# Kernel tuning notes

Hardware: AMD Instinct MI355X
Metric: run time of the kernel (lower is better)

Reference implementation:

```python
import jax, jax.numpy as jnp
import numpy as np

H = 1024        # bridge_hidden_dim
NH = 16         # num_attention_heads
HD = H // NH    # head_dim = 64
B, S = 4, 1024
PHYS_W = 0.2
CONS_W = 0.15


def setup_inputs() -> dict:
    key = jax.random.key(0)
    ks = jax.random.split(key, 16)
    sc = 0.02
    return {
        "cnn_features": jax.random.normal(ks[0], (B, S, H), jnp.float32),
        "llm_features": jax.random.normal(ks[1], (B, S, H), jnp.float32),
        "Wq": jax.random.normal(ks[2], (H, H), jnp.float32) * sc,
        "bq": jnp.zeros((H,), jnp.float32),
        "Wk": jax.random.normal(ks[3], (H, H), jnp.float32) * sc,
        "bk": jnp.zeros((H,), jnp.float32),
        "Wv": jax.random.normal(ks[4], (H, H), jnp.float32) * sc,
        "bv": jnp.zeros((H,), jnp.float32),
        "Wo": jax.random.normal(ks[5], (H, H), jnp.float32) * sc,
        "bo": jnp.zeros((H,), jnp.float32),
        "ln_g": jnp.ones((H,), jnp.float32),
        "ln_b": jnp.zeros((H,), jnp.float32),
        "e_energy": jax.random.normal(ks[6], (H,), jnp.float32),
        "e_mass": jax.random.normal(ks[7], (H,), jnp.float32),
        "e_momentum": jax.random.normal(ks[8], (H,), jnp.float32),
    }


def _layernorm(x, g, b, eps=1e-5):
    mu = jnp.mean(x, axis=-1, keepdims=True)
    var = jnp.var(x, axis=-1, keepdims=True)
    return (x - mu) * jax.lax.rsqrt(var + eps) * g + b


def _split_heads(x):
    b, s, _ = x.shape
    return x.reshape(b, s, NH, HD).transpose(0, 2, 1, 3)  # [b, h, s, d]


def _physics_attention(q_in, k_in, v_in, Wq, bq, Wk, bk, Wv, bv, Wo, bo, ln_g, ln_b):
    # q_in: [b, sq, H]; k_in == v_in: [b, sk, H] with sq == sk (required by bias math)
    Q = _split_heads(q_in @ Wq.T + bq)  # [b,h,s,d]
    K = _split_heads(k_in @ Wk.T + bk)
    V = _split_heads(v_in @ Wv.T + bv)
    scores = jnp.einsum('bhqd,bhkd->bhqk', Q, K) / jnp.sqrt(jnp.float32(HD))
    # physics constraints (broadcast [b,h,s,1] over key axis)
    energy_bias = jnp.sum(Q * K, axis=-1, keepdims=True) * PHYS_W
    mass_bias = jnp.mean(Q + K, axis=-1, keepdims=True) * CONS_W
    scores = scores + energy_bias + mass_bias
    attn = jax.nn.softmax(scores, axis=-1)  # dropout is identity in eval
    att = jnp.einsum('bhqk,bhkd->bhqd', attn, V)
    b, h, s, d = att.shape
    att = att.transpose(0, 2, 1, 3).reshape(b, s, h * d)
    out = att @ Wo.T + bo
    return _layernorm(q_in + out, ln_g, ln_b)


def reference(cnn_features, llm_features, Wq, bq, Wk, bk, Wv, bv, Wo, bo,
              ln_g, ln_b, e_energy, e_mass, e_momentum):
    b = cnn_features.shape[0]
    phys = jnp.stack([e_energy, e_mass, e_momentum], axis=0)  # [3, H]
    phys = jnp.broadcast_to(phys[None], (b, 3, H))
    aug_cnn = jnp.concatenate([cnn_features, phys], axis=1)  # [b, S+3, H]
    aug_llm = jnp.concatenate([llm_features, phys], axis=1)
    cnn_att = _physics_attention(aug_cnn, aug_llm, aug_llm,
                                 Wq, bq, Wk, bk, Wv, bv, Wo, bo, ln_g, ln_b)
    llm_att = _physics_attention(aug_llm, aug_cnn, aug_cnn,
                                 Wq, bq, Wk, bk, Wv, bv, Wo, bo, ln_g, ln_b)
    cnn_out = cnn_att[:, :cnn_features.shape[1], :]
    llm_out = llm_att[:, :llm_features.shape[1], :]
    return (cnn_out, llm_out)
```

## Files before the change

### kernel.cpp

```cpp
#include <hip/hip_runtime.h>
#include <stdint.h>

#define SA 1027
#define SPAD 1088

typedef __attribute__((ext_vector_type(8))) short short8;
typedef __attribute__((ext_vector_type(4))) float f32x4;
typedef __attribute__((ext_vector_type(2))) unsigned int u32x2;

typedef const __attribute__((address_space(1))) uint8_t* gas1;
typedef __attribute__((address_space(3))) uint8_t* las3;

__device__ __forceinline__ void gload16(const void* g, void* l){
  __builtin_amdgcn_global_load_lds((gas1)g, (las3)l, 16, 0, 0);
}

__device__ __forceinline__ uint16_t f2bf(float f){
  uint32_t x = __builtin_bit_cast(uint32_t, f);
  x = (x + 0x7fffu + ((x >> 16) & 1u)) >> 16;
  return (uint16_t)x;
}
__device__ __forceinline__ float bf2f(uint16_t u){
  uint32_t x = ((uint32_t)u) << 16;
  return __builtin_bit_cast(float, x);
}

__device__ __forceinline__ f32x4 mfma16(short8 a, short8 b, f32x4 c){
  return __builtin_amdgcn_mfma_f32_16x16x32_bf16(a, b, c, 0, 0, 0);
}

#define QSCALE 0.18033688011112042f

__global__ __launch_bounds__(256) void prep_wb(
    const float* __restrict__ Wq, const float* __restrict__ Wk,
    const float* __restrict__ Wv, const float* __restrict__ Wo,
    const float* __restrict__ bq, const float* __restrict__ bk,
    const float* __restrict__ bv, const float* __restrict__ bo,
    uint16_t* __restrict__ W, float* __restrict__ bias){
  const int gid = blockIdx.x*256 + threadIdx.x;
  if (gid < 1048576){
    const int w = gid >> 18;
    const int off = (gid & 262143) << 2;
    const float* src = (w==0) ? Wq : (w==1) ? Wk : (w==2) ? Wv : Wo;
    const float4 v = *(const float4*)(src + off);
    ushort4 u;
    u.x = f2bf(v.x); u.y = f2bf(v.y); u.z = f2bf(v.z); u.w = f2bf(v.w);
    *(ushort4*)(W + ((size_t)w << 20) + off) = u;
  } else if (gid < 1048576 + 1024){
    const int i = (gid - 1048576) << 2;
    const int w = i >> 10;
    const int off = i & 1023;
    const float* src = (w==0) ? bq : (w==1) ? bk : (w==2) ? bv : bo;
    *(float4*)(bias + i) = *(const float4*)(src + off);
  }
}

__global__ __launch_bounds__(256) void prep_X(
    const float* __restrict__ cnn, const float* __restrict__ llm,
    uint16_t* __restrict__ X){
  const int row = blockIdx.x*2 + (threadIdx.x >> 7);
  const int c8 = (threadIdx.x & 127) << 3;
  const int cb = row >> 10, s = row & 1023;
  const int c = cb >> 2, b = cb & 3;
  const float* src = (c ? llm : cnn) + ((size_t)(b*1024 + s))*1024 + c8;
  const float4 v0 = *(const float4*)src;
  const float4 v1 = *(const float4*)(src + 4);
  short8 u;
  u[0]=(short)f2bf(v0.x); u[1]=(short)f2bf(v0.y); u[2]=(short)f2bf(v0.z); u[3]=(short)f2bf(v0.w);
  u[4]=(short)f2bf(v1.x); u[5]=(short)f2bf(v1.y); u[6]=(short)f2bf(v1.z); u[7]=(short)f2bf(v1.w);
  *(short8*)(X + (size_t)row*1024 + c8) = u;
}

__global__ __launch_bounds__(256) void phys_qkv(
    const float* __restrict__ ee, const float* __restrict__ em,
    const float* __restrict__ ep, const uint16_t* __restrict__ W,
    const float* __restrict__ bias, uint16_t* __restrict__ Yqk,
    uint16_t* __restrict__ Vt){
  __shared__ float xs[1024];
  const int t = blockIdx.x >> 3;
  const int col = 1024 + (blockIdx.x & 7)*256 + threadIdx.x;
  const float* e = (t==0) ? ee : (t==1) ? em : ep;
  for (int k = threadIdx.x; k < 1024; k += 256) xs[k] = bf2f(f2bf(e[k]));
  __syncthreads();
  const uint16_t* wr = W + (size_t)col*1024;
  float acc = 0.f;
  for (int k = 0; k < 1024; k += 8){
    const short8 w8 = *(const short8*)(wr + k);
    #pragma unroll
    for (int u = 0; u < 8; ++u) acc += bf2f((uint16_t)w8[u]) * xs[k+u];
  }
  const uint16_t o = f2bf(acc + bias[col]);
  if (col < 2048){
    #pragma unroll
    for (int cb = 0; cb < 8; ++cb)
      Yqk[((size_t)cb*SA + 1024 + t)*2048 + col] = o;
  } else {
    const int hd = col - 2048;
    #pragma unroll
    for (int cb = 0; cb < 8; ++cb)
      Vt[((size_t)(cb*1024 + hd))*SPAD + 1024 + t] = o;
  }
}

__global__ __launch_bounds__(512, 2) void qkv192(
    const uint16_t* __restrict__ A, const uint16_t* __restrict__ B,
    const float* __restrict__ bias, uint16_t* __restrict__ Yqk,
    uint16_t* __restrict__ Vt){
  extern __shared__ uint8_t lds[];
  const int tid = threadIdx.x;
  const int lane = tid & 63, wid = tid >> 6;
  const int l15 = lane & 15, l4 = lane >> 4;
  const int wm = wid >> 2, wn = wid & 3;
  const int wg = (blockIdx.x & 7)*64 + (blockIdx.x >> 3);
  const int bm = wg >> 4, bn = wg & 15;

  const uint16_t* Ag = A + (size_t)bm*256*1024;
  const uint16_t* Bg = B + (size_t)bn*192*1024;

  const int srow8 = lane >> 3;
  const int gch = (lane & 7) ^ srow8;
  const int c0 = wid*2, c1 = c0 + 1;
  const size_t ga0 = (size_t)(c0*8 + srow8)*1024 + gch*8;
  const size_t ga1 = (size_t)(c1*8 + srow8)*1024 + gch*8;
  const size_t gb0 = (size_t)((wid*3+0)*8 + srow8)*1024 + gch*8;
  const size_t gb1 = (size_t)((wid*3+1)*8 + srow8)*1024 + gch*8;
  const size_t gb2 = (size_t)((wid*3+2)*8 + srow8)*1024 + gch*8;

#define STG_A(buf, H, kt) do { \
    gload16(Ag + (size_t)(H)*131072 + (size_t)(kt)*64 + ga0, lds + (buf)*57344 + (H)*16384 + c0*1024); \
    gload16(Ag + (size_t)(H)*131072 + (size_t)(kt)*64 + ga1, lds + (buf)*57344 + (H)*16384 + c1*1024); \
  } while(0)
#define STG_B(buf, kt) do { \
    gload16(Bg + (size_t)(kt)*64 + gb0, lds + (buf)*57344 + 32768 + (wid*3+0)*1024); \
    gload16(Bg + (size_t)(kt)*64 + gb1, lds + (buf)*57344 + 32768 + (wid*3+1)*1024); \
    gload16(Bg + (size_t)(kt)*64 + gb2, lds + (buf)*57344 + 32768 + (wid*3+2)*1024); \
  } while(0)

  int koff[2];
  koff[0] = (l4*16) ^ ((l15 & 7) << 4);
  koff[1] = (64 + l4*16) ^ ((l15 & 7) << 4);
  const int arow = (wm*128 + l15) * 128;
  const int bbase = 32768 + (wn*48 + l15) * 128;

  f32x4 acc[8][3];
  #pragma unroll
  for (int i = 0; i < 8; ++i)
    #pragma unroll
    for (int j = 0; j < 3; ++j) acc[i][j] = (f32x4){0.f,0.f,0.f,0.f};

  const int NT = 16;
  STG_A(0,0,0); STG_A(0,1,0); STG_B(0,0); STG_B(1,1);
  asm volatile("s_waitcnt vmcnt(3)" ::: "memory");
  __builtin_amdgcn_s_barrier();

  for (int s = 0; s < NT; ++s){
    const int b = s & 1, nb = b ^ 1;
    const uint8_t* L = lds + b*57344;
    short8 af[4][2], af2[4][2], bfr[3][2];

    if (s+1 < NT){ STG_A(nb, 0, s+1); STG_A(nb, 1, s+1); }
    #pragma unroll
    for (int i = 0; i < 4; ++i){
      af[i][0] = *(const short8*)(L + arow + i*2048 + koff[0]);
      af[i][1] = *(const short8*)(L + arow + i*2048 + koff[1]);
    }
    #pragma unroll
    for (int j = 0; j < 3; ++j){
      bfr[j][0] = *(const short8*)(L + bbase + j*2048 + koff[0]);
      bfr[j][1] = *(const short8*)(L + bbase + j*2048 + koff[1]);
    }
    __builtin_amdgcn_s_barrier();
    asm volatile("s_waitcnt lgkmcnt(0)" ::: "memory");
    __builtin_amdgcn_s_setprio(1);
    #pragma unroll
    for (int i = 0; i < 4; ++i)
      #pragma unroll
      for (int j = 0; j < 3; ++j)
        acc[i][j] = mfma16(af[i][1], bfr[j][1], mfma16(af[i][0], bfr[j][0], acc[i][j]));
    __builtin_amdgcn_s_setprio(0);
    __builtin_amdgcn_s_barrier();

    if (s+2 < NT){ STG_B(b, s+2); }
    #pragma unroll
    for (int i = 0; i < 4; ++i){
      af2[i][0] = *(const short8*)(L + arow + 8192 + i*2048 + koff[0]);
      af2[i][1] = *(const short8*)(L + arow + 8192 + i*2048 + koff[1]);
    }
    __builtin_amdgcn_s_barrier();
    asm volatile("s_waitcnt lgkmcnt(0)" ::: "memory");
    __builtin_amdgcn_s_setprio(1);
    #pragma unroll
    for (int i = 0; i < 4; ++i)
      #pragma unroll
      for (int j = 0; j < 3; ++j)
        acc[i+4][j] = mfma16(af2[i][1], bfr[j][1], mfma16(af2[i][0], bfr[j][0], acc[i+4][j]));
    __builtin_amdgcn_s_setprio(0);
    if (s < NT-2)       asm volatile("s_waitcnt vmcnt(3)" ::: "memory");
    else if (s == NT-2) asm volatile("s_waitcnt vmcnt(0)" ::: "memory");
    __builtin_amdgcn_s_barrier();
  }

  #pragma unroll
  for (int j = 0; j < 3; ++j){
    const int n = bn*192 + wn*48 + j*16 + l15;
    const float bb = bias[n];
    if (n < 2048){
      const float sc = (n < 1024) ? QSCALE : 1.0f;
      #pragma unroll
      for (int i = 0; i < 8; ++i){
        const int m0 = bm*256 + wm*128 + i*16 + l4*4;
        #pragma unroll
        for (int r = 0; r < 4; ++r){
          const int m = m0 + r;
          Yqk[((size_t)(m >> 10)*SA + (m & 1023))*2048 + n] = f2bf((acc[i][j][r] + bb) * sc);
        }
      }
    } else {
      const int hd = n - 2048;
      #pragma unroll
      for (int i = 0; i < 8; ++i){
        const int m0 = bm*256 + wm*128 + i*16 + l4*4;
        const size_t vrow = (size_t)(m0 >> 10)*1024 + hd;
        const uint32_t w0 = (uint32_t)f2bf(acc[i][j][0] + bb) | ((uint32_t)f2bf(acc[i][j][1] + bb) << 16);
        const uint32_t w1 = (uint32_t)f2bf(acc[i][j][2] + bb) | ((uint32_t)f2bf(acc[i][j][3] + bb) << 16);
        *(u32x2*)(Vt + vrow*SPAD + (m0 & 1023)) = (u32x2){w0, w1};
      }
    }
  }
#undef STG_A
#undef STG_B
}

__global__ __launch_bounds__(512, 2) void oproj256(
    const uint16_t* __restrict__ A, const uint16_t* __restrict__ B,
    const float* __restrict__ bias, uint16_t* __restrict__ C){
  extern __shared__ uint8_t lds[];
  const int tid = threadIdx.x;
  const int lane = tid & 63, wid = tid >> 6;
  const int l15 = lane & 15, l4 = lane >> 4;
  const int wm = wid >> 2, wn = wid & 3;
  const int wg = (blockIdx.x & 7)*32 + (blockIdx.x >> 3);
  const int bm = wg >> 3, bn = wg & 7;

  const uint16_t* Ag = A + (size_t)bm*256*1024;
  const uint16_t* Bg = B + (size_t)bn*128*1024;

  const int srow8 = lane >> 3;
  const int gch = (lane & 7) ^ srow8;
  const int c0 = wid*2, c1 = c0 + 1;
  const size_t ga0 = (size_t)(c0*8 + srow8)*1024 + gch*8;
  const size_t ga1 = (size_t)(c1*8 + srow8)*1024 + gch*8;

#define STG_A(buf, H, kt) do { \
    gload16(Ag + (size_t)(H)*131072 + (size_t)(kt)*64 + ga0, lds + (buf)*49152 + (H)*16384 + c0*1024); \
    gload16(Ag + (size_t)(H)*131072 + (size_t)(kt)*64 + ga1, lds + (buf)*49152 + (H)*16384 + c1*1024); \
  } while(0)
#define STG_B(buf, kt) do { \
    gload16(Bg + (size_t)(kt)*64 + ga0, lds + (buf)*49152 + 32768 + c0*1024); \
    gload16(Bg + (size_t)(kt)*64 + ga1, lds + (buf)*49152 + 32768 + c1*1024); \
  } while(0)

  int koff[2];
  koff[0] = (l4*16) ^ ((l15 & 7) << 4);
  koff[1] = (64 + l4*16) ^ ((l15 & 7) << 4);
  const int abase = wm*16384 + l15*128;
  const int bbase = 32768 + (wn*32 + l15)*128;

  f32x4 acc[8][2];
  #pragma unroll
  for (int i = 0; i < 8; ++i){ acc[i][0] = (f32x4){0,0,0,0}; acc[i][1] = (f32x4){0,0,0,0}; }

  const int NT = 16;
  STG_A(0,0,0); STG_A(0,1,0); STG_B(0,0); STG_B(1,1);
  asm volatile("s_waitcnt vmcnt(2)" ::: "memory");
  __builtin_amdgcn_s_barrier();

  for (int s = 0; s < NT; ++s){
    const int b = s & 1, nb = b ^ 1;
    const uint8_t* L = lds + b*49152;
    short8 af[4][2], af2[4][2], bfr[2][2];

    if (s+1 < NT){ STG_A(nb, 0, s+1); }
    #pragma unroll
    for (int i = 0; i < 4; ++i){
      af[i][0] = *(const short8*)(L + abase + i*2048 + koff[0]);
      af[i][1] = *(const short8*)(L + abase + i*2048 + koff[1]);
    }
    #pragma unroll
    for (int j = 0; j < 2; ++j){
      bfr[j][0] = *(const short8*)(L + bbase + j*2048 + koff[0]);
      bfr[j][1] = *(const short8*)(L + bbase + j*2048 + koff[1]);
    }
    __builtin_amdgcn_s_barrier();
    asm volatile("s_waitcnt lgkmcnt(0)" ::: "memory");
    __builtin_amdgcn_s_setprio(1);
    #pragma unroll
    for (int i = 0; i < 4; ++i)
      #pragma unroll
      for (int j = 0; j < 2; ++j)
        acc[i][j] = mfma16(af[i][1], bfr[j][1], mfma16(af[i][0], bfr[j][0], acc[i][j]));
    __builtin_amdgcn_s_setprio(0);
    __builtin_amdgcn_s_barrier();

    if (s+1 < NT){ STG_A(nb, 1, s+1); }
    if (s+2 < NT){ STG_B(b, s+2); }
    #pragma unroll
    for (int i = 0; i < 4; ++i){
      af2[i][0] = *(const short8*)(L + abase + 8192 + i*2048 + koff[0]);
      af2[i][1] = *(const short8*)(L + abase + 8192 + i*2048 + koff[1]);
    }
    __builtin_amdgcn_s_barrier();
    asm volatile("s_waitcnt lgkmcnt(0)" ::: "memory");
    __builtin_amdgcn_s_setprio(1);
    #pragma unroll
    for (int i = 0; i < 4; ++i)
      #pragma unroll
      for (int j = 0; j < 2; ++j)
        acc[i+4][j] = mfma16(af2[i][1], bfr[j][1], mfma16(af2[i][0], bfr[j][0], acc[i+4][j]));
    __builtin_amdgcn_s_setprio(0);
    if (s < NT-2)       asm volatile("s_waitcnt vmcnt(2)" ::: "memory");
    else if (s == NT-2) asm volatile("s_waitcnt vmcnt(0)" ::: "memory");
    __builtin_amdgcn_s_barrier();
  }

  #pragma unroll
  for (int j = 0; j < 2; ++j){
    const int n = bn*128 + wn*32 + j*16 + l15;
    const float bb = bias[n];
    #pragma unroll
    for (int i = 0; i < 8; ++i){
      const size_t m0 = (size_t)bm*256 + wm*128 + i*16 + l4*4;
      #pragma unroll
      for (int r = 0; r < 4; ++r)
        C[(m0 + r)*1024 + n] = f2bf(acc[i][j][r] + bb);
    }
  }
#undef STG_A
#undef STG_B
}

__global__ __launch_bounds__(512, 4) void attn_k(
    const uint16_t* __restrict__ Yqk, const uint16_t* __restrict__ Vt,
    uint16_t* __restrict__ att){
  extern __shared__ uint8_t lds[];
  const int tid = threadIdx.x;
  const int lane = tid & 63, wid = tid >> 6;
  const int l15 = lane & 15, l4 = lane >> 4;
  const int i = blockIdx.x;
  const int inst = (i & 7)*16 + ((i >> 3) & 15);
  const int qb = i >> 7;
  const int h = inst & 15, cb = inst >> 4;
  const size_t yrow0 = (size_t)cb * SA;
  const int q0 = qb*256 + wid*32;
  const size_t vbase = (size_t)inst * 64 * SPAD;
  const uint16_t* Yk = Yqk + yrow0*2048 + 1024 + h*64;

  short8 qf[2][2];
  #pragma unroll
  for (int u = 0; u < 2; ++u){
    const uint16_t* p = Yqk + (yrow0 + q0 + u*16 + l15)*2048 + h*64 + l4*8;
    qf[u][0] = *(const short8*)p;
    qf[u][1] = *(const short8*)(p + 32);
  }

  f32x4 o0[4], o1[4];
  float psum0 = 0.f, psum1 = 0.f;
  #pragma unroll
  for (int d = 0; d < 4; ++d){ o0[d] = (f32x4){0,0,0,0}; o1[d] = (f32x4){0,0,0,0}; }

  int koff[2], koffp[2], pwo[4];
  #pragma unroll
  for (int kk = 0; kk < 2; ++kk){
    koff[kk]  = (l15*128 + kk*64 + l4*16) ^ ((l15 & 7) << 4);
    koffp[kk] = l15*144 + kk*64 + l4*16;
  }
  #pragma unroll
  for (int nt = 0; nt < 4; ++nt)
    pwo[nt] = l15*144 + nt*32 + l4*8;
  uint8_t* const pb = lds + 49152 + wid*2304;

  const int srow = lane >> 3, schunk = lane & 7;
  const int strow = wid*8 + srow;
  const int sgch = schunk ^ srow;

#define ASTAGE(t3, kt) do { \
    gload16(Yk + (size_t)((kt)*64 + strow)*2048 + sgch*8, lds + (t3)*8192 + wid*1024); \
    gload16(Vt + vbase + (size_t)strow*SPAD + (kt)*64 + sgch*8, lds + 24576 + (t3)*8192 + wid*1024); \
  } while(0)

  ASTAGE(0, 0);
  ASTAGE(1, 1);
  asm volatile("s_waitcnt vmcnt(2)" ::: "memory");
  __builtin_amdgcn_s_barrier();

  for (int kt = 0; kt < 17; ++kt){
    const int c3 = kt % 3;
    if (kt <= 14){ const int t3 = (kt + 2) % 3; ASTAGE(t3, kt + 2); }
    const uint8_t* bK = lds + c3*8192;
    const uint8_t* bV = lds + 24576 + c3*8192;

    f32x4 sa[4], sb[4];
    #pragma unroll
    for (int nt = 0; nt < 4; ++nt){
      const short8 k0 = *(const short8*)(bK + nt*2048 + koff[0]);
      const short8 k1 = *(const short8*)(bK + nt*2048 + koff[1]);
      sa[nt] = mfma16(k1, qf[0][1], mfma16(k0, qf[0][0], (f32x4){0,0,0,0}));
      sb[nt] = mfma16(k1, qf[1][1], mfma16(k0, qf[1][0], (f32x4){0,0,0,0}));
    }
    if (kt == 16){
      #pragma unroll
      for (int nt = 0; nt < 4; ++nt)
        #pragma unroll
        for (int r = 0; r < 4; ++r){
          if (nt*16 + l4*4 + r >= 3){ sa[nt][r] = -3e38f; sb[nt][r] = -3e38f; }
        }
    }
    #pragma unroll
    for (int nt = 0; nt < 4; ++nt){
      const float p0 = __builtin_amdgcn_exp2f(sa[nt][0]);
      const float p1 = __builtin_amdgcn_exp2f(sa[nt][1]);
      const float p2 = __builtin_amdgcn_exp2f(sa[nt][2]);
      const float p3 = __builtin_amdgcn_exp2f(sa[nt][3]);
      psum0 += (p0 + p1) + (p2 + p3);
      uint32_t w0, w1;
      asm("v_cvt_pk_bf16_f32 %0, %1, %2" : "=v"(w0) : "v"(p0), "v"(p1));
      asm("v_cvt_pk_bf16_f32 %0, %1, %2" : "=v"(w1) : "v"(p2), "v"(p3));
      *(u32x2*)(pb + pwo[nt]) = (u32x2){w0, w1};
    }
    short8 vf[4][2];
    #pragma unroll
    for (int dt = 0; dt < 4; ++dt){
      vf[dt][0] = *(const short8*)(bV + dt*2048 + koff[0]);
      vf[dt][1] = *(const short8*)(bV + dt*2048 + koff[1]);
    }
    #pragma unroll
    for (int kk = 0; kk < 2; ++kk){
      const short8 pf = *(const short8*)(pb + koffp[kk]);
      #pragma unroll
      for (int dt = 0; dt < 4; ++dt)
        o0[dt] = mfma16(pf, vf[dt][kk], o0[dt]);
    }
    #pragma unroll
    for (int nt = 0; nt < 4; ++nt){
      const float p0 = __builtin_amdgcn_exp2f(sb[nt][0]);
      const float p1 = __builtin_amdgcn_exp2f(sb[nt][1]);
      const float p2 = __builtin_amdgcn_exp2f(sb[nt][2]);
      const float p3 = __builtin_amdgcn_exp2f(sb[nt][3]);
      psum1 += (p0 + p1) + (p2 + p3);
      uint32_t w0, w1;
      asm("v_cvt_pk_bf16_f32 %0, %1, %2" : "=v"(w0) : "v"(p0), "v"(p1));
      asm("v_cvt_pk_bf16_f32 %0, %1, %2" : "=v"(w1) : "v"(p2), "v"(p3));
      *(u32x2*)(pb + pwo[nt]) = (u32x2){w0, w1};
    }
    #pragma unroll
    for (int kk = 0; kk < 2; ++kk){
      const short8 pf = *(const short8*)(pb + koffp[kk]);
      #pragma unroll
      for (int dt = 0; dt < 4; ++dt)
        o1[dt] = mfma16(pf, vf[dt][kk], o1[dt]);
    }
    if (kt <= 14)      asm volatile("s_waitcnt vmcnt(2)" ::: "memory");
    else if (kt == 15) asm volatile("s_waitcnt vmcnt(0)" ::: "memory");
    if (kt <= 15) __builtin_amdgcn_s_barrier();
  }
#undef ASTAGE

  psum0 += __shfl_xor(psum0, 16); psum0 += __shfl_xor(psum0, 32);
  psum1 += __shfl_xor(psum1, 16); psum1 += __shfl_xor(psum1, 32);
  const size_t arow0 = (size_t)cb*1024 + q0;
  #pragma unroll
  for (int r = 0; r < 4; ++r){
    const float inv0 = 1.f / __shfl(psum0, l4*4 + r);
    const float inv1 = 1.f / __shfl(psum1, l4*4 + r);
    #pragma unroll
    for (int dt = 0; dt < 4; ++dt){
      att[(arow0 + l4*4 + r)*1024 + h*64 + dt*16 + l15] = f2bf(o0[dt][r] * inv0);
      att[(arow0 + 16 + l4*4 + r)*1024 + h*64 + dt*16 + l15] = f2bf(o1[dt][r] * inv1);
    }
  }
}

__global__ __launch_bounds__(256) void ln_out(
    const uint16_t* __restrict__ Op, const float* __restrict__ cnn,
    const float* __restrict__ llm, const float* __restrict__ g,
    const float* __restrict__ b, float* __restrict__ out){
  const int row = blockIdx.x;
  const int c = row >> 12, bq = row & 4095;
  const int tid = threadIdx.x;
  const ushort4 u = *(const ushort4*)(Op + (size_t)row*1024 + (tid<<2));
  const float4 rv = *(const float4*)((c ? llm : cnn) + (size_t)bq*1024 + (tid<<2));
  const float x0 = bf2f(u.x) + rv.x;
  const float x1 = bf2f(u.y) + rv.y;
  const float x2 = bf2f(u.z) + rv.z;
  const float x3 = bf2f(u.w) + rv.w;
  float s1 = x0+x1+x2+x3;
  float s2 = x0*x0+x1*x1+x2*x2+x3*x3;
  #pragma unroll
  for (int m=1;m<64;m<<=1){ s1 += __shfl_xor(s1,m); s2 += __shfl_xor(s2,m); }
  __shared__ float r1[4], r2[4];
  const int wid = tid >> 6, lane = tid & 63;
  if (lane == 0){ r1[wid] = s1; r2[wid] = s2; }
  __syncthreads();
  s1 = r1[0]+r1[1]+r1[2]+r1[3];
  s2 = r2[0]+r2[1]+r2[2]+r2[3];
  const float mu = s1 * 0.0009765625f;
  const float var = s2 * 0.0009765625f - mu*mu;
  const float rs = rsqrtf(var + 1e-5f);
  const float4 gv = *(const float4*)(g + (tid<<2));
  const float4 bv = *(const float4*)(b + (tid<<2));
  float4 ov;
  ov.x = (x0 - mu)*rs*gv.x + bv.x;
  ov.y = (x1 - mu)*rs*gv.y + bv.y;
  ov.z = (x2 - mu)*rs*gv.z + bv.z;
  ov.w = (x3 - mu)*rs*gv.w + bv.w;
  *(float4*)(out + ((size_t)c << 22) + (size_t)bq*1024 + (tid<<2)) = ov;
}

extern "C" void kernel_launch(void* const* d_in, const int* in_sizes, int n_in,
                              void* d_out, int out_size, void* d_ws, size_t ws_size,
                              hipStream_t stream){
  const float* cnn = (const float*)d_in[0];
  const float* llm = (const float*)d_in[1];
  const float* Wq  = (const float*)d_in[2];
  const float* bq  = (const float*)d_in[3];
  const float* Wk  = (const float*)d_in[4];
  const float* bk  = (const float*)d_in[5];
  const float* Wv  = (const float*)d_in[6];
  const float* bv  = (const float*)d_in[7];
  const float* Wo  = (const float*)d_in[8];
  const float* bo  = (const float*)d_in[9];
  const float* lng = (const float*)d_in[10];
  const float* lnb = (const float*)d_in[11];
  const float* ee  = (const float*)d_in[12];
  const float* em  = (const float*)d_in[13];
  const float* ep  = (const float*)d_in[14];

  uint8_t* ws = (uint8_t*)d_ws;
  uint16_t* X    = (uint16_t*)(ws + 0);
  uint16_t* W    = (uint16_t*)(ws + 16777216);
  float*    bias = (float*)   (ws + 25165824);
  uint16_t* Yqk  = (uint16_t*)(ws + 25182208);
  uint16_t* Vt   = (uint16_t*)(ws + 59785216);
  uint16_t* att  = X;
  uint16_t* Op   = Yqk;
  float* out = (float*)d_out;

  hipFuncSetAttribute((const void*)qkv192,
                      hipFuncAttributeMaxDynamicSharedMemorySize, 114688);
  hipFuncSetAttribute((const void*)oproj256,
                      hipFuncAttributeMaxDynamicSharedMemorySize, 98304);
  hipFuncSetAttribute((const void*)attn_k,
                      hipFuncAttributeMaxDynamicSharedMemorySize, 67584);

  prep_wb<<<4100, 256, 0, stream>>>(Wq, Wk, Wv, Wo, bq, bk, bv, bo, W, bias);
  prep_X<<<4096, 256, 0, stream>>>(cnn, llm, X);
  phys_qkv<<<24, 256, 0, stream>>>(ee, em, ep, W, bias, Yqk, Vt);
  qkv192<<<512, 512, 114688, stream>>>(X, W, bias, Yqk, Vt);
  attn_k<<<512, 512, 67584, stream>>>(Yqk, Vt, att);
  oproj256<<<256, 512, 98304, stream>>>(att, W + 3145728, bias + 3072, Op);
  ln_out<<<8192, 256, 0, stream>>>(Op, cnn, llm, lng, lnb, out);
}
```

Measured before the change: 175.5 us.

## Merge prep kernels into one launch and halve GEMM M-tiles to 128 rows

Combines weight conversion, input conversion and the physics-token QKV projection into a single prep kernel. The physics projection now reads fp32 weights directly, so it no longer depends on the converted bf16 weights. The QKV and output-projection GEMMs shrink their M tile from 256 to 128 rows, which halves LDS and accumulator use so launch bounds can target 4 blocks per CU, and doubles the grid. This trades fewer launches and higher occupancy for less operand reuse per tile and more global traffic for the B matrix.

```diff
diff --git a/kernel.cpp b/kernel.cpp
--- a/kernel.cpp
+++ b/kernel.cpp
@@ -31,78 +31,80 @@
 
 #define QSCALE 0.18033688011112042f
 
-__global__ __launch_bounds__(256) void prep_wb(
+__global__ __launch_bounds__(256) void prep_all(
+    const float* __restrict__ cnn, const float* __restrict__ llm,
     const float* __restrict__ Wq, const float* __restrict__ Wk,
     const float* __restrict__ Wv, const float* __restrict__ Wo,
     const float* __restrict__ bq, const float* __restrict__ bk,
     const float* __restrict__ bv, const float* __restrict__ bo,
-    uint16_t* __restrict__ W, float* __restrict__ bias){
-  const int gid = blockIdx.x*256 + threadIdx.x;
-  if (gid < 1048576){
-    const int w = gid >> 18;
-    const int off = (gid & 262143) << 2;
-    const float* src = (w==0) ? Wq : (w==1) ? Wk : (w==2) ? Wv : Wo;
-    const float4 v = *(const float4*)(src + off);
-    ushort4 u;
-    u.x = f2bf(v.x); u.y = f2bf(v.y); u.z = f2bf(v.z); u.w = f2bf(v.w);
-    *(ushort4*)(W + ((size_t)w << 20) + off) = u;
-  } else if (gid < 1048576 + 1024){
-    const int i = (gid - 1048576) << 2;
-    const int w = i >> 10;
-    const int off = i & 1023;
-    const float* src = (w==0) ? bq : (w==1) ? bk : (w==2) ? bv : bo;
-    *(float4*)(bias + i) = *(const float4*)(src + off);
-  }
-}
-
-__global__ __launch_bounds__(256) void prep_X(
-    const float* __restrict__ cnn, const float* __restrict__ llm,
-    uint16_t* __restrict__ X){
-  const int row = blockIdx.x*2 + (threadIdx.x >> 7);
-  const int c8 = (threadIdx.x & 127) << 3;
-  const int cb = row >> 10, s = row & 1023;
-  const int c = cb >> 2, b = cb & 3;
-  const float* src = (c ? llm : cnn) + ((size_t)(b*1024 + s))*1024 + c8;
-  const float4 v0 = *(const float4*)src;
-  const float4 v1 = *(const float4*)(src + 4);
-  short8 u;
-  u[0]=(short)f2bf(v0.x); u[1]=(short)f2bf(v0.y); u[2]=(short)f2bf(v0.z); u[3]=(short)f2bf(v0.w);
-  u[4]=(short)f2bf(v1.x); u[5]=(short)f2bf(v1.y); u[6]=(short)f2bf(v1.z); u[7]=(short)f2bf(v1.w);
-  *(short8*)(X + (size_t)row*1024 + c8) = u;
-}
-
-__global__ __launch_bounds__(256) void phys_qkv(
     const float* __restrict__ ee, const float* __restrict__ em,
-    const float* __restrict__ ep, const uint16_t* __restrict__ W,
-    const float* __restrict__ bias, uint16_t* __restrict__ Yqk,
+    const float* __restrict__ ep,
+    uint16_t* __restrict__ W, float* __restrict__ bias,
+    uint16_t* __restrict__ X, uint16_t* __restrict__ Yqk,
     uint16_t* __restrict__ Vt){
-  __shared__ float xs[1024];
-  const int t = blockIdx.x >> 3;
-  const int col = 1024 + (blockIdx.x & 7)*256 + threadIdx.x;
-  const float* e = (t==0) ? ee : (t==1) ? em : ep;
-  for (int k = threadIdx.x; k < 1024; k += 256) xs[k] = bf2f(f2bf(e[k]));
-  __syncthreads();
-  const uint16_t* wr = W + (size_t)col*1024;
-  float acc = 0.f;
-  for (int k = 0; k < 1024; k += 8){
-    const short8 w8 = *(const short8*)(wr + k);
-    #pragma unroll
-    for (int u = 0; u < 8; ++u) acc += bf2f((uint16_t)w8[u]) * xs[k+u];
-  }
-  const uint16_t o = f2bf(acc + bias[col]);
-  if (col < 2048){
-    #pragma unroll
-    for (int cb = 0; cb < 8; ++cb)
-      Yqk[((size_t)cb*SA + 1024 + t)*2048 + col] = o;
+  const int bid = blockIdx.x;
+  if (bid < 4100){
+    const int gid = bid*256 + threadIdx.x;
+    if (gid < 1048576){
+      const int w = gid >> 18;
+      const int off = (gid & 262143) << 2;
+      const float* src = (w==0) ? Wq : (w==1) ? Wk : (w==2) ? Wv : Wo;
+      const float4 v = *(const float4*)(src + off);
+      ushort4 u;
+      u.x = f2bf(v.x); u.y = f2bf(v.y); u.z = f2bf(v.z); u.w = f2bf(v.w);
+      *(ushort4*)(W + ((size_t)w << 20) + off) = u;
+    } else if (gid < 1048576 + 1024){
+      const int i = (gid - 1048576) << 2;
+      const int w = i >> 10;
+      const int off = i & 1023;
+      const float* src = (w==0) ? bq : (w==1) ? bk : (w==2) ? bv : bo;
+      *(float4*)(bias + i) = *(const float4*)(src + off);
+    }
+  } else if (bid < 8196){
+    const int rb = bid - 4100;
+    const int row = rb*2 + (threadIdx.x >> 7);
+    const int c8 = (threadIdx.x & 127) << 3;
+    const int cb = row >> 10, s = row & 1023;
+    const int c = cb >> 2, b = cb & 3;
+    const float* src = (c ? llm : cnn) + ((size_t)(b*1024 + s))*1024 + c8;
+    const float4 v0 = *(const float4*)src;
+    const float4 v1 = *(const float4*)(src + 4);
+    short8 u;
+    u[0]=(short)f2bf(v0.x); u[1]=(short)f2bf(v0.y); u[2]=(short)f2bf(v0.z); u[3]=(short)f2bf(v0.w);
+    u[4]=(short)f2bf(v1.x); u[5]=(short)f2bf(v1.y); u[6]=(short)f2bf(v1.z); u[7]=(short)f2bf(v1.w);
+    *(short8*)(X + (size_t)row*1024 + c8) = u;
   } else {
-    const int hd = col - 2048;
-    #pragma unroll
-    for (int cb = 0; cb < 8; ++cb)
-      Vt[((size_t)(cb*1024 + hd))*SPAD + 1024 + t] = o;
-  }
-}
-
-__global__ __launch_bounds__(512, 2) void qkv192(
+    __shared__ float xs[1024];
+    const int pb = bid - 8196;
+    const int t = pb >> 3;
+    const int col = 1024 + (pb & 7)*256 + threadIdx.x;
+    const float* e = (t==0) ? ee : (t==1) ? em : ep;
+    for (int k = threadIdx.x; k < 1024; k += 256) xs[k] = bf2f(f2bf(e[k]));
+    __syncthreads();
+    const float* wrow = (col < 2048) ? (Wk + (size_t)(col-1024)*1024)
+                                     : (Wv + (size_t)(col-2048)*1024);
+    const float bb = (col < 2048) ? bk[col-1024] : bv[col-2048];
+    float acc = 0.f;
+    for (int k = 0; k < 1024; k += 4){
+      const float4 w4 = *(const float4*)(wrow + k);
+      acc += bf2f(f2bf(w4.x))*xs[k] + bf2f(f2bf(w4.y))*xs[k+1]
+           + bf2f(f2bf(w4.z))*xs[k+2] + bf2f(f2bf(w4.w))*xs[k+3];
+    }
+    const uint16_t o = f2bf(acc + bb);
+    if (col < 2048){
+      #pragma unroll
+      for (int cb = 0; cb < 8; ++cb)
+        Yqk[((size_t)cb*SA + 1024 + t)*2048 + col] = o;
+    } else {
+      const int hd = col - 2048;
+      #pragma unroll
+      for (int cb = 0; cb < 8; ++cb)
+        Vt[((size_t)(cb*1024 + hd))*SPAD + 1024 + t] = o;
+    }
+  }
+}
+
+__global__ __launch_bounds__(512, 4) void qkv128(
     const uint16_t* __restrict__ A, const uint16_t* __restrict__ B,
     const float* __restrict__ bias, uint16_t* __restrict__ Yqk,
     uint16_t* __restrict__ Vt){
@@ -111,10 +113,10 @@
   const int lane = tid & 63, wid = tid >> 6;
   const int l15 = lane & 15, l4 = lane >> 4;
   const int wm = wid >> 2, wn = wid & 3;
-  const int wg = (blockIdx.x & 7)*64 + (blockIdx.x >> 3);
+  const int wg = (blockIdx.x & 7)*128 + (blockIdx.x >> 3);
   const int bm = wg >> 4, bn = wg & 15;
 
-  const uint16_t* Ag = A + (size_t)bm*256*1024;
+  const uint16_t* Ag = A + (size_t)bm*128*1024;
   const uint16_t* Bg = B + (size_t)bn*192*1024;
 
   const int srow8 = lane >> 3;
@@ -126,41 +128,41 @@
   const size_t gb1 = (size_t)((wid*3+1)*8 + srow8)*1024 + gch*8;
   const size_t gb2 = (size_t)((wid*3+2)*8 + srow8)*1024 + gch*8;
 
-#define STG_A(buf, H, kt) do { \
-    gload16(Ag + (size_t)(H)*131072 + (size_t)(kt)*64 + ga0, lds + (buf)*57344 + (H)*16384 + c0*1024); \
-    gload16(Ag + (size_t)(H)*131072 + (size_t)(kt)*64 + ga1, lds + (buf)*57344 + (H)*16384 + c1*1024); \
+#define STG_A(buf, kt) do { \
+    gload16(Ag + (size_t)(kt)*64 + ga0, lds + (buf)*40960 + c0*1024); \
+    gload16(Ag + (size_t)(kt)*64 + ga1, lds + (buf)*40960 + c1*1024); \
   } while(0)
 #define STG_B(buf, kt) do { \
-    gload16(Bg + (size_t)(kt)*64 + gb0, lds + (buf)*57344 + 32768 + (wid*3+0)*1024); \
-    gload16(Bg + (size_t)(kt)*64 + gb1, lds + (buf)*57344 + 32768 + (wid*3+1)*1024); \
-    gload16(Bg + (size_t)(kt)*64 + gb2, lds + (buf)*57344 + 32768 + (wid*3+2)*1024); \
+    gload16(Bg + (size_t)(kt)*64 + gb0, lds + (buf)*40960 + 16384 + (wid*3+0)*1024); \
+    gload16(Bg + (size_t)(kt)*64 + gb1, lds + (buf)*40960 + 16384 + (wid*3+1)*1024); \
+    gload16(Bg + (size_t)(kt)*64 + gb2, lds + (buf)*40960 + 16384 + (wid*3+2)*1024); \
   } while(0)
 
   int koff[2];
   koff[0] = (l4*16) ^ ((l15 & 7) << 4);
   koff[1] = (64 + l4*16) ^ ((l15 & 7) << 4);
-  const int arow = (wm*128 + l15) * 128;
-  const int bbase = 32768 + (wn*48 + l15) * 128;
-
-  f32x4 acc[8][3];
-  #pragma unroll
-  for (int i = 0; i < 8; ++i)
+  const int arow = (wm*64 + l15) * 128;
+  const int bbase = 16384 + (wn*48 + l15) * 128;
+
+  f32x4 acc[4][3];
+  #pragma unroll
+  for (int i = 0; i < 4; ++i)
     #pragma unroll
     for (int j = 0; j < 3; ++j) acc[i][j] = (f32x4){0.f,0.f,0.f,0.f};
 
   const int NT = 16;
-  STG_A(0,0,0); STG_A(0,1,0); STG_B(0,0); STG_B(1,1);
+  STG_A(0,0); STG_B(0,0); STG_B(1,1);
   asm volatile("s_waitcnt vmcnt(3)" ::: "memory");
   __builtin_amdgcn_s_barrier();
 
   for (int s = 0; s < NT; ++s){
     const int b = s & 1, nb = b ^ 1;
-    const uint8_t* L = lds + b*57344;
-    short8 af[4][2], af2[4][2], bfr[3][2];
-
-    if (s+1 < NT){ STG_A(nb, 0, s+1); STG_A(nb, 1, s+1); }
-    #pragma unroll
-    for (int i = 0; i < 4; ++i){
+    const uint8_t* L = lds + b*40960;
+    short8 af[2][2], af2[2][2], bfr[3][2];
+
+    if (s+1 < NT){ STG_A(nb, s+1); }
+    #pragma unroll
+    for (int i = 0; i < 2; ++i){
       af[i][0] = *(const short8*)(L + arow + i*2048 + koff[0]);
       af[i][1] = *(const short8*)(L + arow + i*2048 + koff[1]);
     }
@@ -173,7 +175,7 @@
     asm volatile("s_waitcnt lgkmcnt(0)" ::: "memory");
     __builtin_amdgcn_s_setprio(1);
     #pragma unroll
-    for (int i = 0; i < 4; ++i)
+    for (int i = 0; i < 2; ++i)
       #pragma unroll
       for (int j = 0; j < 3; ++j)
         acc[i][j] = mfma16(af[i][1], bfr[j][1], mfma16(af[i][0], bfr[j][0], acc[i][j]));
@@ -182,18 +184,18 @@
 
     if (s+2 < NT){ STG_B(b, s+2); }
     #pragma unroll
-    for (int i = 0; i < 4; ++i){
-      af2[i][0] = *(const short8*)(L + arow + 8192 + i*2048 + koff[0]);
-      af2[i][1] = *(const short8*)(L + arow + 8192 + i*2048 + koff[1]);
+    for (int i = 0; i < 2; ++i){
+      af2[i][0] = *(const short8*)(L + arow + 4096 + i*2048 + koff[0]);
+      af2[i][1] = *(const short8*)(L + arow + 4096 + i*2048 + koff[1]);
     }
     __builtin_amdgcn_s_barrier();
     asm volatile("s_waitcnt lgkmcnt(0)" ::: "memory");
     __builtin_amdgcn_s_setprio(1);
     #pragma unroll
-    for (int i = 0; i < 4; ++i)
+    for (int i = 0; i < 2; ++i)
       #pragma unroll
       for (int j = 0; j < 3; ++j)
-        acc[i+4][j] = mfma16(af2[i][1], bfr[j][1], mfma16(af2[i][0], bfr[j][0], acc[i+4][j]));
+        acc[i+2][j] = mfma16(af2[i][1], bfr[j][1], mfma16(af2[i][0], bfr[j][0], acc[i+2][j]));
     __builtin_amdgcn_s_setprio(0);
     if (s < NT-2)       asm volatile("s_waitcnt vmcnt(3)" ::: "memory");
     else if (s == NT-2) asm volatile("s_waitcnt vmcnt(0)" ::: "memory");
@@ -207,8 +209,8 @@
     if (n < 2048){
       const float sc = (n < 1024) ? QSCALE : 1.0f;
       #pragma unroll
-      for (int i = 0; i < 8; ++i){
-        const int m0 = bm*256 + wm*128 + i*16 + l4*4;
+      for (int i = 0; i < 4; ++i){
+        const int m0 = bm*128 + wm*64 + i*16 + l4*4;
         #pragma unroll
         for (int r = 0; r < 4; ++r){
           const int m = m0 + r;
@@ -218,8 +220,8 @@
     } else {
       const int hd = n - 2048;
       #pragma unroll
-      for (int i = 0; i < 8; ++i){
-        const int m0 = bm*256 + wm*128 + i*16 + l4*4;
+      for (int i = 0; i < 4; ++i){
+        const int m0 = bm*128 + wm*64 + i*16 + l4*4;
         const size_t vrow = (size_t)(m0 >> 10)*1024 + hd;
         const uint32_t w0 = (uint32_t)f2bf(acc[i][j][0] + bb) | ((uint32_t)f2bf(acc[i][j][1] + bb) << 16);
         const uint32_t w1 = (uint32_t)f2bf(acc[i][j][2] + bb) | ((uint32_t)f2bf(acc[i][j][3] + bb) << 16);
@@ -231,7 +233,7 @@
 #undef STG_B
 }
 
-__global__ __launch_bounds__(512, 2) void oproj256(
+__global__ __launch_bounds__(512, 4) void oproj128(
     const uint16_t* __restrict__ A, const uint16_t* __restrict__ B,
     const float* __restrict__ bias, uint16_t* __restrict__ C){
   extern __shared__ uint8_t lds[];
@@ -239,10 +241,10 @@
   const int lane = tid & 63, wid = tid >> 6;
   const int l15 = lane & 15, l4 = lane >> 4;
   const int wm = wid >> 2, wn = wid & 3;
-  const int wg = (blockIdx.x & 7)*32 + (blockIdx.x >> 3);
+  const int wg = (blockIdx.x & 7)*64 + (blockIdx.x >> 3);
   const int bm = wg >> 3, bn = wg & 7;
 
-  const uint16_t* Ag = A + (size_t)bm*256*1024;
+  const uint16_t* Ag = A + (size_t)bm*128*1024;
   const uint16_t* Bg = B + (size_t)bn*128*1024;
 
   const int srow8 = lane >> 3;
@@ -251,40 +253,40 @@
   const size_t ga0 = (size_t)(c0*8 + srow8)*1024 + gch*8;
   const size_t ga1 = (size_t)(c1*8 + srow8)*1024 + gch*8;
 
-#define STG_A(buf, H, kt) do { \
-    gload16(Ag + (size_t)(H)*131072 + (size_t)(kt)*64 + ga0, lds + (buf)*49152 + (H)*16384 + c0*1024); \
-    gload16(Ag + (size_t)(H)*131072 + (size_t)(kt)*64 + ga1, lds + (buf)*49152 + (H)*16384 + c1*1024); \
+#define STG_A(buf, kt) do { \
+    gload16(Ag + (size_t)(kt)*64 + ga0, lds + (buf)*32768 + c0*1024); \
+    gload16(Ag + (size_t)(kt)*64 + ga1, lds + (buf)*32768 + c1*1024); \
   } while(0)
 #define STG_B(buf, kt) do { \
-    gload16(Bg + (size_t)(kt)*64 + ga0, lds + (buf)*49152 + 32768 + c0*1024); \
-    gload16(Bg + (size_t)(kt)*64 + ga1, lds + (buf)*49152 + 32768 + c1*1024); \
+    gload16(Bg + (size_t)(kt)*64 + ga0, lds + (buf)*32768 + 16384 + c0*1024); \
+    gload16(Bg + (size_t)(kt)*64 + ga1, lds + (buf)*32768 + 16384 + c1*1024); \
   } while(0)
 
   int koff[2];
   koff[0] = (l4*16) ^ ((l15 & 7) << 4);
   koff[1] = (64 + l4*16) ^ ((l15 & 7) << 4);
-  const int abase = wm*16384 + l15*128;
-  const int bbase = 32768 + (wn*32 + l15)*128;
-
-  f32x4 acc[8][2];
-  #pragma unroll
-  for (int i = 0; i < 8; ++i){ acc[i][0] = (f32x4){0,0,0,0}; acc[i][1] = (f32x4){0,0,0,0}; }
+  const int arow = (wm*64 + l15) * 128;
+  const int bbase = 16384 + (wn*32 + l15) * 128;
+
+  f32x4 acc[4][2];
+  #pragma unroll
+  for (int i = 0; i < 4; ++i){ acc[i][0] = (f32x4){0,0,0,0}; acc[i][1] = (f32x4){0,0,0,0}; }
 
   const int NT = 16;
-  STG_A(0,0,0); STG_A(0,1,0); STG_B(0,0); STG_B(1,1);
+  STG_A(0,0); STG_B(0,0); STG_B(1,1);
   asm volatile("s_waitcnt vmcnt(2)" ::: "memory");
   __builtin_amdgcn_s_barrier();
 
   for (int s = 0; s < NT; ++s){
     const int b = s & 1, nb = b ^ 1;
-    const uint8_t* L = lds + b*49152;
-    short8 af[4][2], af2[4][2], bfr[2][2];
-
-    if (s+1 < NT){ STG_A(nb, 0, s+1); }
-    #pragma unroll
-    for (int i = 0; i < 4; ++i){
-      af[i][0] = *(const short8*)(L + abase + i*2048 + koff[0]);
-      af[i][1] = *(const short8*)(L + abase + i*2048 + koff[1]);
+    const uint8_t* L = lds + b*32768;
+    short8 af[2][2], af2[2][2], bfr[2][2];
+
+    if (s+1 < NT){ STG_A(nb, s+1); }
+    #pragma unroll
+    for (int i = 0; i < 2; ++i){
+      af[i][0] = *(const short8*)(L + arow + i*2048 + koff[0]);
+      af[i][1] = *(const short8*)(L + arow + i*2048 + koff[1]);
     }
     #pragma unroll
     for (int j = 0; j < 2; ++j){
@@ -295,28 +297,27 @@
     asm volatile("s_waitcnt lgkmcnt(0)" ::: "memory");
     __builtin_amdgcn_s_setprio(1);
     #pragma unroll
-    for (int i = 0; i < 4; ++i)
+    for (int i = 0; i < 2; ++i)
       #pragma unroll
       for (int j = 0; j < 2; ++j)
         acc[i][j] = mfma16(af[i][1], bfr[j][1], mfma16(af[i][0], bfr[j][0], acc[i][j]));
     __builtin_amdgcn_s_setprio(0);
     __builtin_amdgcn_s_barrier();
 
-    if (s+1 < NT){ STG_A(nb, 1, s+1); }
     if (s+2 < NT){ STG_B(b, s+2); }
     #pragma unroll
-    for (int i = 0; i < 4; ++i){
-      af2[i][0] = *(const short8*)(L + abase + 8192 + i*2048 + koff[0]);
-      af2[i][1] = *(const short8*)(L + abase + 8192 + i*2048 + koff[1]);
+    for (int i = 0; i < 2; ++i){
+      af2[i][0] = *(const short8*)(L + arow + 4096 + i*2048 + koff[0]);
+      af2[i][1] = *(const short8*)(L + arow + 4096 + i*2048 + koff[1]);
     }
     __builtin_amdgcn_s_barrier();
     asm volatile("s_waitcnt lgkmcnt(0)" ::: "memory");
     __builtin_amdgcn_s_setprio(1);
     #pragma unroll
-    for (int i = 0; i < 4; ++i)
+    for (int i = 0; i < 2; ++i)
       #pragma unroll
       for (int j = 0; j < 2; ++j)
-        acc[i+4][j] = mfma16(af2[i][1], bfr[j][1], mfma16(af2[i][0], bfr[j][0], acc[i+4][j]));
+        acc[i+2][j] = mfma16(af2[i][1], bfr[j][1], mfma16(af2[i][0], bfr[j][0], acc[i+2][j]));
     __builtin_amdgcn_s_setprio(0);
     if (s < NT-2)       asm volatile("s_waitcnt vmcnt(2)" ::: "memory");
     else if (s == NT-2) asm volatile("s_waitcnt vmcnt(0)" ::: "memory");
@@ -328,8 +329,8 @@
     const int n = bn*128 + wn*32 + j*16 + l15;
     const float bb = bias[n];
     #pragma unroll
-    for (int i = 0; i < 8; ++i){
-      const size_t m0 = (size_t)bm*256 + wm*128 + i*16 + l4*4;
+    for (int i = 0; i < 4; ++i){
+      const size_t m0 = (size_t)bm*128 + wm*64 + i*16 + l4*4;
       #pragma unroll
       for (int r = 0; r < 4; ++r)
         C[(m0 + r)*1024 + n] = f2bf(acc[i][j][r] + bb);
@@ -545,18 +546,17 @@
   uint16_t* Op   = Yqk;
   float* out = (float*)d_out;
 
-  hipFuncSetAttribute((const void*)qkv192,
-                      hipFuncAttributeMaxDynamicSharedMemorySize, 114688);
-  hipFuncSetAttribute((const void*)oproj256,
-                      hipFuncAttributeMaxDynamicSharedMemorySize, 98304);
+  hipFuncSetAttribute((const void*)qkv128,
+                      hipFuncAttributeMaxDynamicSharedMemorySize, 81920);
+  hipFuncSetAttribute((const void*)oproj128,
+                      hipFuncAttributeMaxDynamicSharedMemorySize, 65536);
   hipFuncSetAttribute((const void*)attn_k,
                       hipFuncAttributeMaxDynamicSharedMemorySize, 67584);
 
-  prep_wb<<<4100, 256, 0, stream>>>(Wq, Wk, Wv, Wo, bq, bk, bv, bo, W, bias);
-  prep_X<<<4096, 256, 0, stream>>>(cnn, llm, X);
-  phys_qkv<<<24, 256, 0, stream>>>(ee, em, ep, W, bias, Yqk, Vt);
-  qkv192<<<512, 512, 114688, stream>>>(X, W, bias, Yqk, Vt);
+  prep_all<<<8220, 256, 0, stream>>>(cnn, llm, Wq, Wk, Wv, Wo, bq, bk, bv, bo,
+                                     ee, em, ep, W, bias, X, Yqk, Vt);
+  qkv128<<<1024, 512, 81920, stream>>>(X, W, bias, Yqk, Vt);
   attn_k<<<512, 512, 67584, stream>>>(Yqk, Vt, att);
-  oproj256<<<256, 512, 98304, stream>>>(att, W + 3145728, bias + 3072, Op);
+  oproj128<<<512, 512, 65536, stream>>>(att, W + 3145728, bias + 3072, Op);
   ln_out<<<8192, 256, 0, stream>>>(Op, cnn, llm, lng, lnb, out);
 }
```

New measurement: 180.3 us. 2.8% more time.
